# Performance work log

Measured on AMD Instinct MI355X. Metric: run time of the kernel, lower is better.

Reference implementation:

```python
import jax, jax.numpy as jnp
import numpy as np

HIDDEN = 4096
INTER = 14336
TOKENS = 4096


def setup_inputs() -> dict:
    key = jax.random.key(0)
    k_x, k_g, k_u, k_d = jax.random.split(key, 4)
    scale_in = 1.0 / np.sqrt(HIDDEN)
    scale_mid = 1.0 / np.sqrt(INTER)
    return {
        "x": jax.random.normal(k_x, (TOKENS, HIDDEN), dtype=jnp.float32),
        "w_gate": jax.random.normal(k_g, (HIDDEN, INTER), dtype=jnp.float32) * scale_in,
        "w_up": jax.random.normal(k_u, (HIDDEN, INTER), dtype=jnp.float32) * scale_in,
        "w_down": jax.random.normal(k_d, (INTER, HIDDEN), dtype=jnp.float32) * scale_mid,
    }


def reference(x, w_gate, w_up, w_down):
    # SwiGLU: down( silu(x @ Wg) * (x @ Wu) )
    gate = jax.nn.silu(jnp.einsum("td,df->tf", x, w_gate))  # [T, INTER]
    up = jnp.einsum("td,df->tf", x, w_up)                   # [T, INTER]
    return jnp.einsum("tf,fd->td", gate * up, w_down)       # [T, HIDDEN]
```

## Files before the change

kernel.cpp:

```cpp
#include <hip/hip_runtime.h>

#define H_DIM 4096
#define I_DIM 14336
#define T_DIM 4096
#define N2    (2*I_DIM)

typedef float  f32x4  __attribute__((ext_vector_type(4)));
typedef float  f32x2  __attribute__((ext_vector_type(2)));
typedef unsigned int u32x4 __attribute__((ext_vector_type(4)));
typedef unsigned int u32x2 __attribute__((ext_vector_type(2)));
typedef __bf16 bf16x8 __attribute__((ext_vector_type(8)));
typedef unsigned short u16;

__device__ __forceinline__ unsigned int pack2bf(float a, float b){
  unsigned int ua = __builtin_bit_cast(unsigned int, a);
  unsigned int ub = __builtin_bit_cast(unsigned int, b);
  ua = (ua + 0x7fffu + ((ua >> 16) & 1u)) >> 16;
  ub = (ub + 0x7fffu + ((ub >> 16) & 1u)) >> 16;
  return (ua & 0xffffu) | (ub << 16);
}
__device__ __forceinline__ u16 f2bf(float a){
  unsigned int u = __builtin_bit_cast(unsigned int, a);
  u = (u + 0x7fffu + ((u >> 16) & 1u)) >> 16;
  return (u16)u;
}
__device__ __forceinline__ bf16x8 lds_frag(const unsigned char* p){
  u32x4 v = *(const u32x4*)p;
  return __builtin_bit_cast(bf16x8, v);
}

#define GLOAD16(g, l) __builtin_amdgcn_global_load_lds( \
    (const __attribute__((address_space(1))) unsigned int*)(g), \
    (__attribute__((address_space(3))) unsigned int*)(l), 16, 0, 0)

#define WAITVM0  asm volatile("s_waitcnt vmcnt(0)" ::: "memory")
#define CFENCE   asm volatile("" ::: "memory")

__global__ __launch_bounds__(256)
void k_cast(const float* __restrict__ in, u16* __restrict__ out, long n)
{
  long i = ((long)blockIdx.x * 256 + threadIdx.x) * 8;
  if (i >= n) return;
  f32x4 a = *(const f32x4*)(in + i);
  f32x4 b = *(const f32x4*)(in + i + 4);
  u32x4 o = { pack2bf(a[0],a[1]), pack2bf(a[2],a[3]),
              pack2bf(b[0],b[1]), pack2bf(b[2],b[3]) };
  *(u32x4*)(out + i) = o;
}

__global__ __launch_bounds__(256)
void k_transpose(const float* __restrict__ in, u16* __restrict__ out,
                 int R, int C, int remap)
{
  __shared__ u16 tile[64][68];
  const int tid = threadIdx.x;
  const int r0 = blockIdx.x * 64, c0 = blockIdx.y * 64;
  const int lr  = tid >> 4;
  const int lc4 = (tid & 15) * 4;
  #pragma unroll
  for (int s = 0; s < 4; ++s){
    f32x4 v = *(const f32x4*)(in + (size_t)(r0 + lr + s*16) * C + c0 + lc4);
    #pragma unroll
    for (int j = 0; j < 4; ++j) tile[lc4 + j][lr + s*16] = f2bf(v[j]);
  }
  __syncthreads();
  #pragma unroll
  for (int s = 0; s < 4; ++s){
    int cl = lr + s*16;
    int n  = c0 + cl;
    int orow = (remap < 0) ? n : (((n >> 4) << 5) + (n & 15) + remap);
    u32x2 v = *(const u32x2*)&tile[cl][lc4];
    *(u32x2*)(out + (size_t)orow * R + r0 + lc4) = v;
  }
}

template<int EPI>
__global__ __launch_bounds__(512, 2)
void gemm8p(const u16* __restrict__ A, const u16* __restrict__ B,
            void* __restrict__ Cout, const int K, const int ldc,
            const int mblocks)
{
  __shared__ unsigned char smem[131072];
  const int tid  = threadIdx.x;
  const int lane = tid & 63;
  const int wid  = tid >> 6;
  const int wm   = wid >> 2;
  const int wn   = wid & 3;

  const int nwg = gridDim.x;
  const int cpx = nwg >> 3;
  const int bid = blockIdx.x;
  const int swz = (bid & 7) * cpx + (bid >> 3);
  const int m0 = (swz % mblocks) << 8;
  const int n0 = (swz / mblocks) << 8;
  const int NT = K >> 6;

  const int srow = tid >> 3;
  const int gl   = (tid & 7) ^ (srow & 7);
  const u16* Ap = A + (size_t)(m0 + srow) * K + gl * 8;
  const u16* Bp = B + (size_t)(n0 + srow) * K + gl * 8;
  unsigned char* ldsw = smem + tid * 16;
  const size_t rowK64  = (size_t)64 * K;
  const size_t rowK128 = (size_t)128 * K;

  const int r15 = lane & 15;
  const int lhi = lane >> 4;
  const int gk0 = (((r15 >> 2) & 1) << 2) | (lhi ^ (r15 & 3));
  const int gk1 = gk0 ^ 4;
  const unsigned char* ldsr = smem + r15 * 128;

  f32x4 acc[8][4];
  #pragma unroll
  for (int i = 0; i < 8; ++i)
    #pragma unroll
    for (int j = 0; j < 4; ++j) acc[i][j] = (f32x4)0.0f;
  bf16x8 areg[4][2];
  bf16x8 breg[2][2][2];

#define ISSUE(h) do { \
    const int _a = (h) & 3; \
    const size_t _k0 = (size_t)((h) >> 2) << 6; \
    unsigned char* _l = ldsw + (((h) & 7) << 14); \
    const u16* _s = (_a < 2 ? Bp + (size_t)_a * rowK128 \
                            : Ap + (size_t)(_a - 2) * rowK128) + _k0; \
    GLOAD16(_s, _l); \
    GLOAD16(_s + rowK64, _l + 8192); \
  } while (0)

#define RD_A(SLOT, MQ) do { \
    const unsigned char* _b = ldsr + ((SLOT) << 14) + (MQ) * 8192; \
    _Pragma("unroll") \
    for (int _m = 0; _m < 4; ++_m) { \
      areg[_m][0] = lds_frag(_b + _m * 2048 + gk0 * 16); \
      areg[_m][1] = lds_frag(_b + _m * 2048 + gk1 * 16); \
    } \
  } while (0)

#define RD_B(SLOT, NQ) do { \
    const unsigned char* _b = ldsr + ((SLOT) << 14) + (wn & 1) * 8192 + (NQ) * 4096; \
    _Pragma("unroll") \
    for (int _n = 0; _n < 2; ++_n) { \
      breg[NQ][_n][0] = lds_frag(_b + _n * 2048 + gk0 * 16); \
      breg[NQ][_n][1] = lds_frag(_b + _n * 2048 + gk1 * 16); \
    } \
  } while (0)

#define MFMAQ(MQ, NQ) \
    _Pragma("unroll") \
    for (int _m = 0; _m < 4; ++_m) \
      _Pragma("unroll") \
      for (int _n = 0; _n < 2; ++_n) { \
        acc[(MQ)*4+_m][(NQ)*2+_n] = __builtin_amdgcn_mfma_f32_16x16x32_bf16( \
            areg[_m][0], breg[NQ][_n][0], acc[(MQ)*4+_m][(NQ)*2+_n], 0, 0, 0); \
        acc[(MQ)*4+_m][(NQ)*2+_n] = __builtin_amdgcn_mfma_f32_16x16x32_bf16( \
            areg[_m][1], breg[NQ][_n][1], acc[(MQ)*4+_m][(NQ)*2+_n], 0, 0, 0); \
      }

  #pragma unroll
  for (int h = 0; h < 4; ++h) ISSUE(h);
  WAITVM0;
  __builtin_amdgcn_s_barrier();
  CFENCE;

  for (int t = 0; t < NT; ++t){
    const int bh = t << 2;
    const int sB = (bh + (wn >> 1)) & 7;
    const int sA = (bh + 2 + wm) & 7;
    const bool more = (t + 1 < NT);
    if (more){ ISSUE(bh + 4); ISSUE(bh + 5); ISSUE(bh + 6); ISSUE(bh + 7); }
    RD_A(sA, 0);
    RD_B(sB, 0);
    __builtin_amdgcn_s_setprio(1);
    MFMAQ(0, 0);
    __builtin_amdgcn_s_setprio(0);
    RD_B(sB, 1);
    __builtin_amdgcn_s_setprio(1);
    MFMAQ(0, 1);
    __builtin_amdgcn_s_setprio(0);
    RD_A(sA, 1);
    __builtin_amdgcn_s_setprio(1);
    MFMAQ(1, 1);
    MFMAQ(1, 0);
    __builtin_amdgcn_s_setprio(0);
    if (more) WAITVM0;
    __builtin_amdgcn_s_barrier();
    CFENCE;
  }

#undef ISSUE
#undef RD_A
#undef RD_B
#undef MFMAQ

  const int r0 = lhi * 4;
  if (EPI == 0){
    float* C = (float*)Cout;
    #pragma unroll
    for (int mi = 0; mi < 8; ++mi)
      #pragma unroll
      for (int nj = 0; nj < 4; ++nj)
        #pragma unroll
        for (int j = 0; j < 4; ++j)
          C[(size_t)(m0 + wm*128 + mi*16 + r0 + j) * ldc + n0 + wn*64 + nj*16 + r15] =
            acc[mi][nj][j];
  } else {
    u16* C = (u16*)Cout;
    const int hb = ((n0 + wn*64) >> 1);
    #pragma unroll
    for (int mi = 0; mi < 8; ++mi)
      #pragma unroll
      for (int p = 0; p < 2; ++p)
        #pragma unroll
        for (int j = 0; j < 4; ++j){
          float g = acc[mi][2*p][j];
          float u = acc[mi][2*p+1][j];
          float s = g / (1.0f + __expf(-g));
          C[(size_t)(m0 + wm*128 + mi*16 + r0 + j) * ldc + hb + p*16 + r15] =
            f2bf(s * u);
        }
  }
}

__global__ __launch_bounds__(256, 2)
void k_gateup_fb(const float* __restrict__ x, const float* __restrict__ wg,
                 const float* __restrict__ wu, u16* __restrict__ h)
{
  __shared__ unsigned char smem[61440];
  const int tid  = threadIdx.x;
  const int lane = tid & 63;
  const int wid  = tid >> 6;
  const int wr   = wid >> 1, wc = wid & 1;
  const int m0   = blockIdx.x * 128;
  const int n0   = blockIdx.y * 128;
  const int s_am = tid >> 3;
  const int s_ak = (tid & 7) * 4;
  const int s_bn = (tid & 63) * 2;
  const int s_bk = (tid >> 6) * 8;

  f32x4 accg[4][4], accu[4][4];
  #pragma unroll
  for (int i = 0; i < 4; ++i)
    #pragma unroll
    for (int j = 0; j < 4; ++j){ accg[i][j] = (f32x4)0.0f; accu[i][j] = (f32x4)0.0f; }

  f32x4 pa[4];
  f32x2 pg[8], pu[8];
  auto gload = [&](int kt){
    const int k0 = kt * 32;
    #pragma unroll
    for (int it = 0; it < 4; ++it)
      pa[it] = *(const f32x4*)(x + (size_t)(m0 + it*32 + s_am) * H_DIM + k0 + s_ak);
    #pragma unroll
    for (int r = 0; r < 8; ++r){
      pg[r] = *(const f32x2*)(wg + (size_t)(k0 + s_bk + r) * I_DIM + n0 + s_bn);
      pu[r] = *(const f32x2*)(wu + (size_t)(k0 + s_bk + r) * I_DIM + n0 + s_bn);
    }
  };
  auto sstore = [&](int b){
    unsigned char* Ab = smem + b * 10240;
    #pragma unroll
    for (int it = 0; it < 4; ++it){
      u32x2 v = { pack2bf(pa[it][0], pa[it][1]), pack2bf(pa[it][2], pa[it][3]) };
      *(u32x2*)(Ab + (s_am + it*32) * 80 + s_ak * 2) = v;
    }
    unsigned char* Bg = smem + 20480 + b * 10240;
    unsigned char* Bu = smem + 40960 + b * 10240;
    #pragma unroll
    for (int c = 0; c < 2; ++c){
      u32x4 vg = { pack2bf(pg[0][c], pg[1][c]), pack2bf(pg[2][c], pg[3][c]),
                   pack2bf(pg[4][c], pg[5][c]), pack2bf(pg[6][c], pg[7][c]) };
      *(u32x4*)(Bg + (s_bn + c) * 80 + s_bk * 2) = vg;
      u32x4 vu = { pack2bf(pu[0][c], pu[1][c]), pack2bf(pu[2][c], pu[3][c]),
                   pack2bf(pu[4][c], pu[5][c]), pack2bf(pu[6][c], pu[7][c]) };
      *(u32x4*)(Bu + (s_bn + c) * 80 + s_bk * 2) = vu;
    }
  };
  const int koff = (lane >> 4) * 16;
  const int ar   = wr * 64 + (lane & 15);
  const int br   = wc * 64 + (lane & 15);
  auto compute = [&](int b){
    const unsigned char* Ab = smem + b * 10240;
    const unsigned char* Bg = smem + 20480 + b * 10240;
    const unsigned char* Bu = smem + 40960 + b * 10240;
    bf16x8 a[4];
    #pragma unroll
    for (int mi = 0; mi < 4; ++mi)
      a[mi] = lds_frag(Ab + (ar + mi*16) * 80 + koff);
    #pragma unroll
    for (int nh = 0; nh < 2; ++nh){
      bf16x8 bg[2], bu[2];
      #pragma unroll
      for (int nj = 0; nj < 2; ++nj){
        bg[nj] = lds_frag(Bg + (br + (nh*2+nj)*16) * 80 + koff);
        bu[nj] = lds_frag(Bu + (br + (nh*2+nj)*16) * 80 + koff);
      }
      #pragma unroll
      for (int mi = 0; mi < 4; ++mi)
        #pragma unroll
        for (int nj = 0; nj < 2; ++nj){
          accg[mi][nh*2+nj] = __builtin_amdgcn_mfma_f32_16x16x32_bf16(a[mi], bg[nj], accg[mi][nh*2+nj], 0, 0, 0);
          accu[mi][nh*2+nj] = __builtin_amdgcn_mfma_f32_16x16x32_bf16(a[mi], bu[nj], accu[mi][nh*2+nj], 0, 0, 0);
        }
    }
  };
  gload(0); sstore(0); __syncthreads();
  const int NT = H_DIM / 32;
  for (int kt = 0; kt < NT; ++kt){
    const int b = kt & 1;
    if (kt + 1 < NT) gload(kt + 1);
    compute(b);
    if (kt + 1 < NT) sstore(b ^ 1);
    __syncthreads();
  }
  const int bm = wr * 64 + ((lane >> 4) << 2);
  const int bn = wc * 64 + (lane & 15);
  #pragma unroll
  for (int mi = 0; mi < 4; ++mi)
    #pragma unroll
    for (int ni = 0; ni < 4; ++ni)
      #pragma unroll
      for (int r = 0; r < 4; ++r){
        float gv = accg[mi][ni][r];
        float uv = accu[mi][ni][r];
        float s  = gv / (1.0f + __expf(-gv));
        h[(size_t)(m0 + bm + mi*16 + r) * I_DIM + n0 + bn + ni*16] = f2bf(s * uv);
      }
}

__global__ __launch_bounds__(256, 2)
void k_down_fb(const u16* __restrict__ h, const float* __restrict__ wd,
               float* __restrict__ out)
{
  __shared__ unsigned char smem[40960];
  const int tid  = threadIdx.x;
  const int lane = tid & 63;
  const int wid  = tid >> 6;
  const int wr   = wid >> 1, wc = wid & 1;
  const int m0   = blockIdx.x * 128;
  const int n0   = blockIdx.y * 128;
  const int s_am = tid >> 1;
  const int s_ak = (tid & 1) * 16;
  const int s_bn = (tid & 63) * 2;
  const int s_bk = (tid >> 6) * 8;

  f32x4 acc[4][4];
  #pragma unroll
  for (int i = 0; i < 4; ++i)
    #pragma unroll
    for (int j = 0; j < 4; ++j) acc[i][j] = (f32x4)0.0f;

  u32x4 pha[2];
  f32x2 pb[8];
  auto gload = [&](int kt){
    const int k0 = kt * 32;
    const u16* ap = h + (size_t)(m0 + s_am) * I_DIM + k0 + s_ak;
    pha[0] = *(const u32x4*)(ap);
    pha[1] = *(const u32x4*)(ap + 8);
    #pragma unroll
    for (int r = 0; r < 8; ++r)
      pb[r] = *(const f32x2*)(wd + (size_t)(k0 + s_bk + r) * H_DIM + n0 + s_bn);
  };
  auto sstore = [&](int b){
    unsigned char* Ab = smem + b * 10240;
    *(u32x4*)(Ab + s_am * 80 + s_ak * 2)      = pha[0];
    *(u32x4*)(Ab + s_am * 80 + s_ak * 2 + 16) = pha[1];
    unsigned char* Bb = smem + 20480 + b * 10240;
    #pragma unroll
    for (int c = 0; c < 2; ++c){
      u32x4 v = { pack2bf(pb[0][c], pb[1][c]), pack2bf(pb[2][c], pb[3][c]),
                  pack2bf(pb[4][c], pb[5][c]), pack2bf(pb[6][c], pb[7][c]) };
      *(u32x4*)(Bb + (s_bn + c) * 80 + s_bk * 2) = v;
    }
  };
  const int koff = (lane >> 4) * 16;
  const int ar   = wr * 64 + (lane & 15);
  const int br   = wc * 64 + (lane & 15);
  auto compute = [&](int b){
    const unsigned char* Ab = smem + b * 10240;
    const unsigned char* Bb = smem + 20480 + b * 10240;
    bf16x8 a[4];
    #pragma unroll
    for (int mi = 0; mi < 4; ++mi)
      a[mi] = lds_frag(Ab + (ar + mi*16) * 80 + koff);
    #pragma unroll
    for (int nh = 0; nh < 2; ++nh){
      bf16x8 bb[2];
      #pragma unroll
      for (int nj = 0; nj < 2; ++nj)
        bb[nj] = lds_frag(Bb + (br + (nh*2+nj)*16) * 80 + koff);
      #pragma unroll
      for (int mi = 0; mi < 4; ++mi)
        #pragma unroll
        for (int nj = 0; nj < 2; ++nj)
          acc[mi][nh*2+nj] = __builtin_amdgcn_mfma_f32_16x16x32_bf16(a[mi], bb[nj], acc[mi][nh*2+nj], 0, 0, 0);
    }
  };
  gload(0); sstore(0); __syncthreads();
  const int NT = I_DIM / 32;
  for (int kt = 0; kt < NT; ++kt){
    const int b = kt & 1;
    if (kt + 1 < NT) gload(kt + 1);
    compute(b);
    if (kt + 1 < NT) sstore(b ^ 1);
    __syncthreads();
  }
  const int bm = wr * 64 + ((lane >> 4) << 2);
  const int bn = wc * 64 + (lane & 15);
  #pragma unroll
  for (int mi = 0; mi < 4; ++mi)
    #pragma unroll
    for (int ni = 0; ni < 4; ++ni)
      #pragma unroll
      for (int r = 0; r < 4; ++r)
        out[(size_t)(m0 + bm + mi*16 + r) * H_DIM + n0 + bn + ni*16] = acc[mi][ni][r];
}

extern "C" void kernel_launch(void* const* d_in, const int* in_sizes, int n_in,
                              void* d_out, int out_size, void* d_ws, size_t ws_size,
                              hipStream_t stream)
{
  const float* x  = (const float*)d_in[0];
  const float* wg = (const float*)d_in[1];
  const float* wu = (const float*)d_in[2];
  const float* wd = (const float*)d_in[3];
  float* out = (float*)d_out;

  const size_t X_OFF   = 0;
  const size_t WGU_OFF = 33554432;
  const size_t WD_OFF  = 268435456;
  const size_t H_OFF   = 385875968;
  const size_t NEED    = 503316480;

  if (ws_size >= NEED){
    u16* xb  = (u16*)((char*)d_ws + X_OFF);
    u16* wgu = (u16*)((char*)d_ws + WGU_OFF);
    u16* wdt = (u16*)((char*)d_ws + WD_OFF);
    u16* h   = (u16*)((char*)d_ws + H_OFF);

    long nx = (long)T_DIM * H_DIM;
    k_cast<<<(unsigned)((nx/8 + 255)/256), 256, 0, stream>>>(x, xb, nx);
    dim3 tg(H_DIM/64, I_DIM/64);
    k_transpose<<<tg, 256, 0, stream>>>(wg, wgu, H_DIM, I_DIM, 0);
    k_transpose<<<tg, 256, 0, stream>>>(wu, wgu, H_DIM, I_DIM, 16);
    dim3 td(I_DIM/64, H_DIM/64);
    k_transpose<<<td, 256, 0, stream>>>(wd, wdt, I_DIM, H_DIM, -1);

    gemm8p<1><<<dim3(16 * (N2/256)), dim3(512), 0, stream>>>(
        xb, wgu, h, H_DIM, I_DIM, T_DIM/256);
    gemm8p<0><<<dim3(16 * (H_DIM/256)), dim3(512), 0, stream>>>(
        h, wdt, out, I_DIM, H_DIM, T_DIM/256);
  } else {
    u16* h = (u16*)d_ws;
    size_t maxrows = ws_size / ((size_t)I_DIM * 2);
    int chunk = (int)(maxrows > (size_t)T_DIM ? (size_t)T_DIM : maxrows);
    chunk &= ~127;
    if (chunk < 128) chunk = 128;
    for (int r0 = 0; r0 < T_DIM; r0 += chunk){
      int rows = (T_DIM - r0 < chunk) ? (T_DIM - r0) : chunk;
      dim3 g1(rows / 128, I_DIM / 128);
      dim3 g2(rows / 128, H_DIM / 128);
      k_gateup_fb<<<g1, dim3(256), 0, stream>>>(x + (size_t)r0 * H_DIM, wg, wu, h);
      k_down_fb  <<<g2, dim3(256), 0, stream>>>(h, wd, out + (size_t)r0 * H_DIM);
    }
  }
}
```

Measured before the change: 1.445 ms.

## Switch GEMM core to 32x32x16 bf16 MFMA with matching gate/up interleave

Replaces the 16x16x32 MFMA inner loop with 32x32x16 MFMA tiles, which need fewer LDS fragment reads per FLOP and fewer MFMA instructions. The gate/up weight interleave granularity is changed from 16 to 32 columns so that the fused SiLU epilogue can pair adjacent 32-wide accumulator tiles. The LDS read pattern and the output row/column mapping are rewritten for the 32x32 accumulator layout. This risks LDS bank conflicts under the existing swizzle and less flexible interleaving of loads with MFMAs.

```diff
diff --git a/kernel.cpp b/kernel.cpp
--- a/kernel.cpp
+++ b/kernel.cpp
@@ -7,6 +7,7 @@
 
 typedef float  f32x4  __attribute__((ext_vector_type(4)));
 typedef float  f32x2  __attribute__((ext_vector_type(2)));
+typedef float  f32x16 __attribute__((ext_vector_type(16)));
 typedef unsigned int u32x4 __attribute__((ext_vector_type(4)));
 typedef unsigned int u32x2 __attribute__((ext_vector_type(2)));
 typedef __bf16 bf16x8 __attribute__((ext_vector_type(8)));
@@ -68,7 +69,7 @@
   for (int s = 0; s < 4; ++s){
     int cl = lr + s*16;
     int n  = c0 + cl;
-    int orow = (remap < 0) ? n : (((n >> 4) << 5) + (n & 15) + remap);
+    int orow = (remap < 0) ? n : (((n >> 5) << 6) + (n & 31) + remap);
     u32x2 v = *(const u32x2*)&tile[cl][lc4];
     *(u32x2*)(out + (size_t)orow * R + r0 + lc4) = v;
   }
@@ -76,7 +77,7 @@
 
 template<int EPI>
 __global__ __launch_bounds__(512, 2)
-void gemm8p(const u16* __restrict__ A, const u16* __restrict__ B,
+void gemm32(const u16* __restrict__ A, const u16* __restrict__ B,
             void* __restrict__ Cout, const int K, const int ldc,
             const int mblocks)
 {
@@ -86,6 +87,8 @@
   const int wid  = tid >> 6;
   const int wm   = wid >> 2;
   const int wn   = wid & 3;
+  const int l31  = lane & 31;
+  const int khi  = lane >> 5;
 
   const int nwg = gridDim.x;
   const int cpx = nwg >> 3;
@@ -103,19 +106,9 @@
   const size_t rowK64  = (size_t)64 * K;
   const size_t rowK128 = (size_t)128 * K;
 
-  const int r15 = lane & 15;
-  const int lhi = lane >> 4;
-  const int gk0 = (((r15 >> 2) & 1) << 2) | (lhi ^ (r15 & 3));
-  const int gk1 = gk0 ^ 4;
-  const unsigned char* ldsr = smem + r15 * 128;
-
-  f32x4 acc[8][4];
-  #pragma unroll
-  for (int i = 0; i < 8; ++i)
-    #pragma unroll
-    for (int j = 0; j < 4; ++j) acc[i][j] = (f32x4)0.0f;
-  bf16x8 areg[4][2];
-  bf16x8 breg[2][2][2];
+  f32x16 acc[4][2];
+  #pragma unroll
+  for (int i = 0; i < 4; ++i){ acc[i][0] = (f32x16)0.0f; acc[i][1] = (f32x16)0.0f; }
 
 #define ISSUE(h) do { \
     const int _a = (h) & 3; \
@@ -127,34 +120,25 @@
     GLOAD16(_s + rowK64, _l + 8192); \
   } while (0)
 
-#define RD_A(SLOT, MQ) do { \
-    const unsigned char* _b = ldsr + ((SLOT) << 14) + (MQ) * 8192; \
-    _Pragma("unroll") \
-    for (int _m = 0; _m < 4; ++_m) { \
-      areg[_m][0] = lds_frag(_b + _m * 2048 + gk0 * 16); \
-      areg[_m][1] = lds_frag(_b + _m * 2048 + gk1 * 16); \
-    } \
+#define KSTEP(aBase, bBase, ks) do { \
+    const int _pg = (((ks)*2 + khi) ^ (l31 & 7)) * 16; \
+    bf16x8 _b0 = lds_frag((bBase)          + _pg); \
+    bf16x8 _a0 = lds_frag((aBase)          + _pg); \
+    bf16x8 _a1 = lds_frag((aBase) + 4096   + _pg); \
+    bf16x8 _a2 = lds_frag((aBase) + 8192   + _pg); \
+    bf16x8 _a3 = lds_frag((aBase) + 12288  + _pg); \
+    bf16x8 _b1 = lds_frag((bBase) + 4096   + _pg); \
+    __builtin_amdgcn_s_setprio(1); \
+    acc[0][0] = __builtin_amdgcn_mfma_f32_32x32x16_bf16(_a0, _b0, acc[0][0], 0, 0, 0); \
+    acc[1][0] = __builtin_amdgcn_mfma_f32_32x32x16_bf16(_a1, _b0, acc[1][0], 0, 0, 0); \
+    acc[2][0] = __builtin_amdgcn_mfma_f32_32x32x16_bf16(_a2, _b0, acc[2][0], 0, 0, 0); \
+    acc[3][0] = __builtin_amdgcn_mfma_f32_32x32x16_bf16(_a3, _b0, acc[3][0], 0, 0, 0); \
+    acc[0][1] = __builtin_amdgcn_mfma_f32_32x32x16_bf16(_a0, _b1, acc[0][1], 0, 0, 0); \
+    acc[1][1] = __builtin_amdgcn_mfma_f32_32x32x16_bf16(_a1, _b1, acc[1][1], 0, 0, 0); \
+    acc[2][1] = __builtin_amdgcn_mfma_f32_32x32x16_bf16(_a2, _b1, acc[2][1], 0, 0, 0); \
+    acc[3][1] = __builtin_amdgcn_mfma_f32_32x32x16_bf16(_a3, _b1, acc[3][1], 0, 0, 0); \
+    __builtin_amdgcn_s_setprio(0); \
   } while (0)
-
-#define RD_B(SLOT, NQ) do { \
-    const unsigned char* _b = ldsr + ((SLOT) << 14) + (wn & 1) * 8192 + (NQ) * 4096; \
-    _Pragma("unroll") \
-    for (int _n = 0; _n < 2; ++_n) { \
-      breg[NQ][_n][0] = lds_frag(_b + _n * 2048 + gk0 * 16); \
-      breg[NQ][_n][1] = lds_frag(_b + _n * 2048 + gk1 * 16); \
-    } \
-  } while (0)
-
-#define MFMAQ(MQ, NQ) \
-    _Pragma("unroll") \
-    for (int _m = 0; _m < 4; ++_m) \
-      _Pragma("unroll") \
-      for (int _n = 0; _n < 2; ++_n) { \
-        acc[(MQ)*4+_m][(NQ)*2+_n] = __builtin_amdgcn_mfma_f32_16x16x32_bf16( \
-            areg[_m][0], breg[NQ][_n][0], acc[(MQ)*4+_m][(NQ)*2+_n], 0, 0, 0); \
-        acc[(MQ)*4+_m][(NQ)*2+_n] = __builtin_amdgcn_mfma_f32_16x16x32_bf16( \
-            areg[_m][1], breg[NQ][_n][1], acc[(MQ)*4+_m][(NQ)*2+_n], 0, 0, 0); \
-      }
 
   #pragma unroll
   for (int h = 0; h < 4; ++h) ISSUE(h);
@@ -168,56 +152,45 @@
     const int sA = (bh + 2 + wm) & 7;
     const bool more = (t + 1 < NT);
     if (more){ ISSUE(bh + 4); ISSUE(bh + 5); ISSUE(bh + 6); ISSUE(bh + 7); }
-    RD_A(sA, 0);
-    RD_B(sB, 0);
-    __builtin_amdgcn_s_setprio(1);
-    MFMAQ(0, 0);
-    __builtin_amdgcn_s_setprio(0);
-    RD_B(sB, 1);
-    __builtin_amdgcn_s_setprio(1);
-    MFMAQ(0, 1);
-    __builtin_amdgcn_s_setprio(0);
-    RD_A(sA, 1);
-    __builtin_amdgcn_s_setprio(1);
-    MFMAQ(1, 1);
-    MFMAQ(1, 0);
-    __builtin_amdgcn_s_setprio(0);
+    const unsigned char* aB = smem + (sA << 14) + l31 * 128;
+    const unsigned char* bB = smem + (sB << 14) + (wn & 1) * 8192 + l31 * 128;
+    KSTEP(aB, bB, 0);
+    KSTEP(aB, bB, 1);
+    KSTEP(aB, bB, 2);
+    KSTEP(aB, bB, 3);
     if (more) WAITVM0;
     __builtin_amdgcn_s_barrier();
     CFENCE;
   }
 
 #undef ISSUE
-#undef RD_A
-#undef RD_B
-#undef MFMAQ
-
-  const int r0 = lhi * 4;
+#undef KSTEP
+
   if (EPI == 0){
     float* C = (float*)Cout;
     #pragma unroll
-    for (int mi = 0; mi < 8; ++mi)
-      #pragma unroll
-      for (int nj = 0; nj < 4; ++nj)
+    for (int mt = 0; mt < 4; ++mt)
+      #pragma unroll
+      for (int nt = 0; nt < 2; ++nt)
         #pragma unroll
-        for (int j = 0; j < 4; ++j)
-          C[(size_t)(m0 + wm*128 + mi*16 + r0 + j) * ldc + n0 + wn*64 + nj*16 + r15] =
-            acc[mi][nj][j];
+        for (int rg = 0; rg < 16; ++rg){
+          const int row = m0 + wm*128 + mt*32 + (rg & 3) + 8*(rg >> 2) + 4*khi;
+          const int col = n0 + wn*64 + nt*32 + l31;
+          C[(size_t)row * ldc + col] = acc[mt][nt][rg];
+        }
   } else {
     u16* C = (u16*)Cout;
-    const int hb = ((n0 + wn*64) >> 1);
-    #pragma unroll
-    for (int mi = 0; mi < 8; ++mi)
-      #pragma unroll
-      for (int p = 0; p < 2; ++p)
-        #pragma unroll
-        for (int j = 0; j < 4; ++j){
-          float g = acc[mi][2*p][j];
-          float u = acc[mi][2*p+1][j];
-          float s = g / (1.0f + __expf(-g));
-          C[(size_t)(m0 + wm*128 + mi*16 + r0 + j) * ldc + hb + p*16 + r15] =
-            f2bf(s * u);
-        }
+    const int col = ((n0 + wn*64) >> 1) + l31;
+    #pragma unroll
+    for (int mt = 0; mt < 4; ++mt)
+      #pragma unroll
+      for (int rg = 0; rg < 16; ++rg){
+        const int row = m0 + wm*128 + mt*32 + (rg & 3) + 8*(rg >> 2) + 4*khi;
+        float g = acc[mt][0][rg];
+        float u = acc[mt][1][rg];
+        float s = g / (1.0f + __expf(-g));
+        C[(size_t)row * ldc + col] = f2bf(s * u);
+      }
   }
 }
 
@@ -441,13 +414,13 @@
     k_cast<<<(unsigned)((nx/8 + 255)/256), 256, 0, stream>>>(x, xb, nx);
     dim3 tg(H_DIM/64, I_DIM/64);
     k_transpose<<<tg, 256, 0, stream>>>(wg, wgu, H_DIM, I_DIM, 0);
-    k_transpose<<<tg, 256, 0, stream>>>(wu, wgu, H_DIM, I_DIM, 16);
+    k_transpose<<<tg, 256, 0, stream>>>(wu, wgu, H_DIM, I_DIM, 32);
     dim3 td(I_DIM/64, H_DIM/64);
     k_transpose<<<td, 256, 0, stream>>>(wd, wdt, I_DIM, H_DIM, -1);
 
-    gemm8p<1><<<dim3(16 * (N2/256)), dim3(512), 0, stream>>>(
+    gemm32<1><<<dim3(16 * (N2/256)), dim3(512), 0, stream>>>(
         xb, wgu, h, H_DIM, I_DIM, T_DIM/256);
-    gemm8p<0><<<dim3(16 * (H_DIM/256)), dim3(512), 0, stream>>>(
+    gemm32<0><<<dim3(16 * (H_DIM/256)), dim3(512), 0, stream>>>(
         h, wdt, out, I_DIM, H_DIM, T_DIM/256);
   } else {
     u16* h = (u16*)d_ws;
```

New measurement: 1.616 ms. 11.8% more time.

## Replace 256x256 GEMM with smaller 128x256 double-buffered tile kernel

Applied to the files above, without the earlier changes.

Swaps the 256x256-tile, K=64, 8-slot LDS pipelined GEMM for a 128x256-tile, K=32 kernel with a simple two-stage double buffer in 48KB of shared memory, targeting 4 workgroups per CU instead of 2. The grid doubles and each wave holds half the accumulators. The aim is more occupancy and latency hiding through concurrent workgroups rather than deep software pipelining. In exchange, arithmetic intensity per tile drops, global and LDS traffic per flop rises, and there are twice as many barriers per unit of K.

```diff
diff --git a/kernel.cpp b/kernel.cpp
--- a/kernel.cpp
+++ b/kernel.cpp
@@ -75,12 +75,12 @@
 }
 
 template<int EPI>
-__global__ __launch_bounds__(512, 2)
-void gemm8p(const u16* __restrict__ A, const u16* __restrict__ B,
-            void* __restrict__ Cout, const int K, const int ldc,
-            const int mblocks)
-{
-  __shared__ unsigned char smem[131072];
+__global__ __launch_bounds__(512, 4)
+void gemmd(const u16* __restrict__ A, const u16* __restrict__ B,
+           void* __restrict__ Cout, const int K, const int ldc,
+           const int mblocks)
+{
+  __shared__ unsigned char smem[49152];
   const int tid  = threadIdx.x;
   const int lane = tid & 63;
   const int wid  = tid >> 6;
@@ -91,96 +91,71 @@
   const int cpx = nwg >> 3;
   const int bid = blockIdx.x;
   const int swz = (bid & 7) * cpx + (bid >> 3);
-  const int m0 = (swz % mblocks) << 8;
+  const int m0 = (swz % mblocks) << 7;
   const int n0 = (swz / mblocks) << 8;
-  const int NT = K >> 6;
-
-  const int srow = tid >> 3;
-  const int gl   = (tid & 7) ^ (srow & 7);
+  const int NT = K >> 5;
+
+  const int srow = tid >> 2;
+  const int gl   = (tid & 3) ^ ((tid >> 3) & 3);
   const u16* Ap = A + (size_t)(m0 + srow) * K + gl * 8;
   const u16* Bp = B + (size_t)(n0 + srow) * K + gl * 8;
   unsigned char* ldsw = smem + tid * 16;
-  const size_t rowK64  = (size_t)64 * K;
   const size_t rowK128 = (size_t)128 * K;
 
   const int r15 = lane & 15;
   const int lhi = lane >> 4;
-  const int gk0 = (((r15 >> 2) & 1) << 2) | (lhi ^ (r15 & 3));
-  const int gk1 = gk0 ^ 4;
-  const unsigned char* ldsr = smem + r15 * 128;
-
-  f32x4 acc[8][4];
-  #pragma unroll
-  for (int i = 0; i < 8; ++i)
+  const int off = r15 * 64 + ((lhi ^ ((r15 >> 1) & 3)) << 4);
+
+  f32x4 acc[4][4];
+  #pragma unroll
+  for (int i = 0; i < 4; ++i)
     #pragma unroll
     for (int j = 0; j < 4; ++j) acc[i][j] = (f32x4)0.0f;
-  bf16x8 areg[4][2];
-  bf16x8 breg[2][2][2];
-
-#define ISSUE(h) do { \
-    const int _a = (h) & 3; \
-    const size_t _k0 = (size_t)((h) >> 2) << 6; \
-    unsigned char* _l = ldsw + (((h) & 7) << 14); \
-    const u16* _s = (_a < 2 ? Bp + (size_t)_a * rowK128 \
-                            : Ap + (size_t)(_a - 2) * rowK128) + _k0; \
+
+#define ISSUE(p, u, k0) do { \
+    unsigned char* _l = ldsw + ((p)*3 + (u)) * 8192; \
+    const u16* _s = ((u) == 0 ? Ap : ((u) == 1 ? Bp : Bp + rowK128)) + (k0); \
     GLOAD16(_s, _l); \
-    GLOAD16(_s + rowK64, _l + 8192); \
   } while (0)
 
-#define RD_A(SLOT, MQ) do { \
-    const unsigned char* _b = ldsr + ((SLOT) << 14) + (MQ) * 8192; \
-    _Pragma("unroll") \
-    for (int _m = 0; _m < 4; ++_m) { \
-      areg[_m][0] = lds_frag(_b + _m * 2048 + gk0 * 16); \
-      areg[_m][1] = lds_frag(_b + _m * 2048 + gk1 * 16); \
-    } \
-  } while (0)
-
-#define RD_B(SLOT, NQ) do { \
-    const unsigned char* _b = ldsr + ((SLOT) << 14) + (wn & 1) * 8192 + (NQ) * 4096; \
-    _Pragma("unroll") \
-    for (int _n = 0; _n < 2; ++_n) { \
-      breg[NQ][_n][0] = lds_frag(_b + _n * 2048 + gk0 * 16); \
-      breg[NQ][_n][1] = lds_frag(_b + _n * 2048 + gk1 * 16); \
-    } \
-  } while (0)
-
-#define MFMAQ(MQ, NQ) \
-    _Pragma("unroll") \
-    for (int _m = 0; _m < 4; ++_m) \
-      _Pragma("unroll") \
-      for (int _n = 0; _n < 2; ++_n) { \
-        acc[(MQ)*4+_m][(NQ)*2+_n] = __builtin_amdgcn_mfma_f32_16x16x32_bf16( \
-            areg[_m][0], breg[NQ][_n][0], acc[(MQ)*4+_m][(NQ)*2+_n], 0, 0, 0); \
-        acc[(MQ)*4+_m][(NQ)*2+_n] = __builtin_amdgcn_mfma_f32_16x16x32_bf16( \
-            areg[_m][1], breg[NQ][_n][1], acc[(MQ)*4+_m][(NQ)*2+_n], 0, 0, 0); \
-      }
-
-  #pragma unroll
-  for (int h = 0; h < 4; ++h) ISSUE(h);
+  ISSUE(0, 0, 0); ISSUE(0, 1, 0); ISSUE(0, 2, 0);
   WAITVM0;
   __builtin_amdgcn_s_barrier();
   CFENCE;
 
   for (int t = 0; t < NT; ++t){
-    const int bh = t << 2;
-    const int sB = (bh + (wn >> 1)) & 7;
-    const int sA = (bh + 2 + wm) & 7;
+    const int p = t & 1;
     const bool more = (t + 1 < NT);
-    if (more){ ISSUE(bh + 4); ISSUE(bh + 5); ISSUE(bh + 6); ISSUE(bh + 7); }
-    RD_A(sA, 0);
-    RD_B(sB, 0);
+    const size_t k1 = (size_t)(t + 1) << 5;
+    if (more){ ISSUE(p^1, 0, k1); ISSUE(p^1, 1, k1); ISSUE(p^1, 2, k1); }
+    const unsigned char* base = smem + p * 24576;
+    const unsigned char* aB = base + wm*4096 + off;
+    const unsigned char* bB = base + 8192 + (wn >> 1)*8192 + (wn & 1)*4096 + off;
+    bf16x8 b0 = lds_frag(bB);
+    bf16x8 a0 = lds_frag(aB);
+    bf16x8 a1 = lds_frag(aB + 1024);
+    bf16x8 a2 = lds_frag(aB + 2048);
+    bf16x8 a3 = lds_frag(aB + 3072);
+    bf16x8 b1 = lds_frag(bB + 1024);
+    bf16x8 b2 = lds_frag(bB + 2048);
+    bf16x8 b3 = lds_frag(bB + 3072);
     __builtin_amdgcn_s_setprio(1);
-    MFMAQ(0, 0);
-    __builtin_amdgcn_s_setprio(0);
-    RD_B(sB, 1);
-    __builtin_amdgcn_s_setprio(1);
-    MFMAQ(0, 1);
-    __builtin_amdgcn_s_setprio(0);
-    RD_A(sA, 1);
-    __builtin_amdgcn_s_setprio(1);
-    MFMAQ(1, 1);
-    MFMAQ(1, 0);
+    acc[0][0] = __builtin_amdgcn_mfma_f32_16x16x32_bf16(a0, b0, acc[0][0], 0, 0, 0);
+    acc[1][0] = __builtin_amdgcn_mfma_f32_16x16x32_bf16(a1, b0, acc[1][0], 0, 0, 0);
+    acc[2][0] = __builtin_amdgcn_mfma_f32_16x16x32_bf16(a2, b0, acc[2][0], 0, 0, 0);
+    acc[3][0] = __builtin_amdgcn_mfma_f32_16x16x32_bf16(a3, b0, acc[3][0], 0, 0, 0);
+    acc[0][1] = __builtin_amdgcn_mfma_f32_16x16x32_bf16(a0, b1, acc[0][1], 0, 0, 0);
+    acc[1][1] = __builtin_amdgcn_mfma_f32_16x16x32_bf16(a1, b1, acc[1][1], 0, 0, 0);
+    acc[2][1] = __builtin_amdgcn_mfma_f32_16x16x32_bf16(a2, b1, acc[2][1], 0, 0, 0);
+    acc[3][1] = __builtin_amdgcn_mfma_f32_16x16x32_bf16(a3, b1, acc[3][1], 0, 0, 0);
+    acc[0][2] = __builtin_amdgcn_mfma_f32_16x16x32_bf16(a0, b2, acc[0][2], 0, 0, 0);
+    acc[1][2] = __builtin_amdgcn_mfma_f32_16x16x32_bf16(a1, b2, acc[1][2], 0, 0, 0);
+    acc[2][2] = __builtin_amdgcn_mfma_f32_16x16x32_bf16(a2, b2, acc[2][2], 0, 0, 0);
+    acc[3][2] = __builtin_amdgcn_mfma_f32_16x16x32_bf16(a3, b2, acc[3][2], 0, 0, 0);
+    acc[0][3] = __builtin_amdgcn_mfma_f32_16x16x32_bf16(a0, b3, acc[0][3], 0, 0, 0);
+    acc[1][3] = __builtin_amdgcn_mfma_f32_16x16x32_bf16(a1, b3, acc[1][3], 0, 0, 0);
+    acc[2][3] = __builtin_amdgcn_mfma_f32_16x16x32_bf16(a2, b3, acc[2][3], 0, 0, 0);
+    acc[3][3] = __builtin_amdgcn_mfma_f32_16x16x32_bf16(a3, b3, acc[3][3], 0, 0, 0);
     __builtin_amdgcn_s_setprio(0);
     if (more) WAITVM0;
     __builtin_amdgcn_s_barrier();
@@ -188,34 +163,31 @@
   }
 
 #undef ISSUE
-#undef RD_A
-#undef RD_B
-#undef MFMAQ
 
   const int r0 = lhi * 4;
   if (EPI == 0){
     float* C = (float*)Cout;
     #pragma unroll
-    for (int mi = 0; mi < 8; ++mi)
+    for (int mi = 0; mi < 4; ++mi)
       #pragma unroll
       for (int nj = 0; nj < 4; ++nj)
         #pragma unroll
         for (int j = 0; j < 4; ++j)
-          C[(size_t)(m0 + wm*128 + mi*16 + r0 + j) * ldc + n0 + wn*64 + nj*16 + r15] =
+          C[(size_t)(m0 + wm*64 + mi*16 + r0 + j) * ldc + n0 + wn*64 + nj*16 + r15] =
             acc[mi][nj][j];
   } else {
     u16* C = (u16*)Cout;
     const int hb = ((n0 + wn*64) >> 1);
     #pragma unroll
-    for (int mi = 0; mi < 8; ++mi)
-      #pragma unroll
-      for (int p = 0; p < 2; ++p)
+    for (int mi = 0; mi < 4; ++mi)
+      #pragma unroll
+      for (int p2 = 0; p2 < 2; ++p2)
         #pragma unroll
         for (int j = 0; j < 4; ++j){
-          float g = acc[mi][2*p][j];
-          float u = acc[mi][2*p+1][j];
+          float g = acc[mi][2*p2][j];
+          float u = acc[mi][2*p2+1][j];
           float s = g / (1.0f + __expf(-g));
-          C[(size_t)(m0 + wm*128 + mi*16 + r0 + j) * ldc + hb + p*16 + r15] =
+          C[(size_t)(m0 + wm*64 + mi*16 + r0 + j) * ldc + hb + p2*16 + r15] =
             f2bf(s * u);
         }
   }
@@ -445,10 +417,10 @@
     dim3 td(I_DIM/64, H_DIM/64);
     k_transpose<<<td, 256, 0, stream>>>(wd, wdt, I_DIM, H_DIM, -1);
 
-    gemm8p<1><<<dim3(16 * (N2/256)), dim3(512), 0, stream>>>(
-        xb, wgu, h, H_DIM, I_DIM, T_DIM/256);
-    gemm8p<0><<<dim3(16 * (H_DIM/256)), dim3(512), 0, stream>>>(
-        h, wdt, out, I_DIM, H_DIM, T_DIM/256);
+    gemmd<1><<<dim3(32 * (N2/256)), dim3(512), 0, stream>>>(
+        xb, wgu, h, H_DIM, I_DIM, T_DIM/128);
+    gemmd<0><<<dim3(32 * (H_DIM/256)), dim3(512), 0, stream>>>(
+        h, wdt, out, I_DIM, H_DIM, T_DIM/128);
   } else {
     u16* h = (u16*)d_ws;
     size_t maxrows = ws_size / ((size_t)I_DIM * 2);
```

Measured after the change: 1.804 ms. 24.9% more time.
